# Performance work log

Measured on AMD Instinct MI355X. Metric: run time of the kernel, lower is better.

## Reference

```python
import jax, jax.numpy as jnp
import numpy as np

N = 50000
HEADS = 3
NEG_SLOPE = 0.2


def _add_self_loops(edge_index, num_nodes):
    loops = jnp.arange(num_nodes, dtype=edge_index.dtype)
    return jnp.concatenate([edge_index, jnp.stack([loops, loops])], axis=1)


def _gcn_conv(x, edge_index, W, b):
    # PyG GCNConv: add self loops, symmetric deg^-1/2 normalization.
    ei = _add_self_loops(edge_index, x.shape[0])
    src, dst = ei[0], ei[1]
    deg = jax.ops.segment_sum(jnp.ones_like(dst, dtype=x.dtype), dst, num_segments=x.shape[0])
    dinv = jax.lax.rsqrt(deg)  # deg >= 1 due to self loops
    norm = dinv[src] * dinv[dst]                      # [E']
    xw = x @ W                                        # [N, F_out]
    out = jax.ops.segment_sum(xw[src] * norm[:, None], dst, num_segments=x.shape[0])
    return out + b


def _gat_conv(x, edge_index, W, att_src, att_dst, b):
    # PyG GATConv (concat=True): self loops, per-edge attention, segment softmax.
    n = x.shape[0]
    ei = _add_self_loops(edge_index, n)
    src, dst = ei[0], ei[1]
    h = (x @ W).reshape(n, HEADS, -1)                 # [N, H, C]
    a_s = (h * att_src).sum(-1)                       # [N, H]
    a_d = (h * att_dst).sum(-1)                       # [N, H]
    e = jax.nn.leaky_relu(a_s[src] + a_d[dst], NEG_SLOPE)   # [E', H]
    m = jax.ops.segment_max(e, dst, num_segments=n)   # [N, H] per-dst max
    e = jnp.exp(e - m[dst])
    s = jax.ops.segment_sum(e, dst, num_segments=n)   # [N, H]
    alpha = e / s[dst]                                # [E', H]
    out = jax.ops.segment_sum(h[src] * alpha[:, :, None], dst, num_segments=n)
    return out.reshape(n, -1) + b                     # [N, H*C]


def setup_inputs() -> dict:
    key = jax.random.key(0)
    ks = jax.random.split(key, 9)
    in_ch, out_ch = 256, 64
    hid = 2 * out_ch  # 128
    E = 800000
    x = jax.random.normal(ks[0], (N, in_ch), dtype=jnp.float32)
    edge_index = jax.random.randint(ks[1], (2, E), 0, N, dtype=jnp.int32)
    W1 = jax.random.normal(ks[2], (in_ch, hid), dtype=jnp.float32) / np.sqrt(in_ch)
    b1 = jnp.zeros((hid,), dtype=jnp.float32)
    W2 = jax.random.normal(ks[3], (hid, HEADS * out_ch), dtype=jnp.float32) / np.sqrt(hid)
    att_src = jax.random.normal(ks[4], (HEADS, out_ch), dtype=jnp.float32) / np.sqrt(out_ch)
    att_dst = jax.random.normal(ks[5], (HEADS, out_ch), dtype=jnp.float32) / np.sqrt(out_ch)
    b2 = jnp.zeros((HEADS * out_ch,), dtype=jnp.float32)
    return {"x": x, "edge_index": edge_index, "W1": W1, "b1": b1,
            "W2": W2, "att_src": att_src, "att_dst": att_dst, "b2": b2}


def reference(x, edge_index, W1, b1, W2, att_src, att_dst, b2):
    h = jax.nn.relu(_gcn_conv(x, edge_index, W1, b1))
    # F.dropout(training=False) is identity in eval mode
    h = _gat_conv(h, edge_index, W2, att_src, att_dst, b2)
    return jax.nn.relu(h)
```

## Files before the change

### kernel.cpp

```cpp
#include <hip/hip_runtime.h>
#include <hip/hip_fp16.h>
#include <math.h>

#define NODES    50000
#define IN_CH    256
#define HID      128
#define HEADS    3
#define HC       64
#define OC       (HEADS*HC)
#define NEG_SLOPE 0.2f

typedef _Float16 half8_t __attribute__((ext_vector_type(8)));
typedef _Float16 half4_t __attribute__((ext_vector_type(4)));
typedef float float4_t __attribute__((ext_vector_type(4)));

__device__ __forceinline__ float lrelu(float v) { return v > 0.f ? v : NEG_SLOPE * v; }

__device__ __forceinline__ unsigned fkey(float f) {
    unsigned b = __float_as_uint(f);
    return (b & 0x80000000u) ? ~b : (b | 0x80000000u);
}
__device__ __forceinline__ float fdec(unsigned k) {
    unsigned b = (k & 0x80000000u) ? (k ^ 0x80000000u) : ~k;
    return __uint_as_float(b);
}

__global__ __launch_bounds__(256) void k_hist(const int* __restrict__ dst, int E, int* __restrict__ cnt,
                                              unsigned short* __restrict__ rank,
                                              const float* __restrict__ W1, const float* __restrict__ W2,
                                              _Float16* __restrict__ W1t, _Float16* __restrict__ W2t) {
    int e = blockIdx.x * 256 + threadIdx.x;
    if (e < E) {
        int r = atomicAdd(&cnt[dst[e]], 1);
        rank[e] = (unsigned short)r;
    }
    if (e < IN_CH * HID) {
        int c = e >> 8, k = e & 255;
        W1t[e] = (_Float16)W1[(size_t)k * HID + c];
    } else if (e < IN_CH * HID + HID * OC) {
        int u = e - IN_CH * HID;
        int c = u >> 7, k = u & 127;
        W2t[u] = (_Float16)W2[(size_t)k * OC + c];
    }
}

__global__ __launch_bounds__(1024) void k_scanA(const int* __restrict__ cnt, int* __restrict__ off,
                                                float* __restrict__ dinv, int* __restrict__ bsum, int n) {
    __shared__ int wsums[16];
    int tid = threadIdx.x, lane = tid & 63, wid = tid >> 6;
    int i = blockIdx.x * 1024 + tid;
    int v = (i < n) ? cnt[i] : 0;
    int incl = v;
    #pragma unroll
    for (int d = 1; d < 64; d <<= 1) {
        int t = __shfl_up(incl, d, 64);
        if (lane >= d) incl += t;
    }
    if (lane == 63) wsums[wid] = incl;
    __syncthreads();
    if (tid == 0) {
        int run = 0;
        #pragma unroll
        for (int j = 0; j < 16; j++) { int t = wsums[j]; wsums[j] = run; run += t; }
        bsum[blockIdx.x] = run;
    }
    __syncthreads();
    if (i < n) {
        off[i] = wsums[wid] + incl - v;
        dinv[i] = rsqrtf((float)(v + 1));
    }
}

__global__ __launch_bounds__(64) void k_scanB(const int* __restrict__ bsum, int* __restrict__ bbase,
                                              int* __restrict__ off, int nb, int n) {
    int tid = threadIdx.x;
    int v = (tid < nb) ? bsum[tid] : 0;
    int incl = v;
    #pragma unroll
    for (int d = 1; d < 64; d <<= 1) {
        int t = __shfl_up(incl, d, 64);
        if (tid >= d) incl += t;
    }
    bbase[tid] = incl - v;
    if (tid == 63) off[n] = incl;
}

__global__ __launch_bounds__(256) void k_scanC(int* __restrict__ off, const int* __restrict__ bbase, int n) {
    int i = blockIdx.x * 256 + threadIdx.x;
    if (i < n) off[i] += bbase[i >> 10];
}

__global__ __launch_bounds__(256) void k_fillg1(const int* __restrict__ src, const int* __restrict__ dst, int E,
                                                const int* __restrict__ off, const unsigned short* __restrict__ rank,
                                                unsigned short* __restrict__ csr,
                                                const float* __restrict__ x, const _Float16* __restrict__ W1t,
                                                const float* __restrict__ dinv, _Float16* __restrict__ xwh,
                                                int n, int fillBlocks) {
    if ((int)blockIdx.x < fillBlocks) {
        int e = blockIdx.x * 256 + threadIdx.x;
        if (e < E) {
            int d = dst[e];
            int p = off[d] + (int)rank[e];
            csr[p] = (unsigned short)src[e];
        }
        return;
    }

    int bid = blockIdx.x - fillBlocks;
    int wid = threadIdx.x >> 6, lane = threadIdx.x & 63;
    int lrow = lane & 15, kgrp = lane >> 4;
    int arow = bid * 64 + wid * 16 + lrow;
    bool rv = arow < n;
    const float* xp = x + (size_t)arow * IN_CH + kgrp * 8;

    float4_t acc[8];
    #pragma unroll
    for (int s = 0; s < 8; s++) acc[s] = (float4_t)(0.f);

    #pragma unroll
    for (int kc = 0; kc < IN_CH; kc += 32) {
        float4 a0, a1;
        if (rv) { a0 = *(const float4*)(xp + kc); a1 = *(const float4*)(xp + kc + 4); }
        else { a0 = make_float4(0.f,0.f,0.f,0.f); a1 = a0; }
        half8_t af;
        af[0]=(_Float16)a0.x; af[1]=(_Float16)a0.y; af[2]=(_Float16)a0.z; af[3]=(_Float16)a0.w;
        af[4]=(_Float16)a1.x; af[5]=(_Float16)a1.y; af[6]=(_Float16)a1.z; af[7]=(_Float16)a1.w;
        #pragma unroll
        for (int s = 0; s < 8; s++) {
            const _Float16* bp = W1t + (size_t)(s * 16 + lrow) * IN_CH + kc + kgrp * 8;
            half8_t bf = *(const half8_t*)bp;
            acc[s] = __builtin_amdgcn_mfma_f32_16x16x32_f16(af, bf, acc[s], 0, 0, 0);
        }
    }

    int orow0 = bid * 64 + wid * 16 + kgrp * 4;
    #pragma unroll
    for (int r = 0; r < 4; r++) {
        int orow = orow0 + r;
        if (orow < n) {
            float sc = dinv[orow];
            _Float16* po = xwh + ((size_t)orow << 7) + lrow;
            #pragma unroll
            for (int s = 0; s < 8; s++) po[s * 16] = (_Float16)(sc * acc[s][r]);
        }
    }
}

__global__ __launch_bounds__(256) void k_gcn(const _Float16* __restrict__ xwh, const unsigned short* __restrict__ csr,
                                             const int* __restrict__ off, const float* __restrict__ dinv,
                                             const float* __restrict__ b1, _Float16* __restrict__ hh, int n) {
    int w = (blockIdx.x * 256 + threadIdx.x) >> 6;
    int lane = threadIdx.x & 63;
    if (w >= n) return;
    int egrp = lane >> 4;
    int c8 = (lane & 15) * 8;
    float acc[8];
    #pragma unroll
    for (int j = 0; j < 8; j++) acc[j] = 0.f;

    int beg = off[w], end = off[w + 1];
    int i = beg;
    for (; i + 16 <= end; i += 16) {
        int s0 = csr[i + egrp];
        int s1 = csr[i + 4 + egrp];
        int s2 = csr[i + 8 + egrp];
        int s3 = csr[i + 12 + egrp];
        half8_t v0 = *(const half8_t*)(xwh + ((size_t)s0 << 7) + c8);
        half8_t v1 = *(const half8_t*)(xwh + ((size_t)s1 << 7) + c8);
        half8_t v2 = *(const half8_t*)(xwh + ((size_t)s2 << 7) + c8);
        half8_t v3 = *(const half8_t*)(xwh + ((size_t)s3 << 7) + c8);
        half8_t p01 = v0 + v1;
        half8_t p23 = v2 + v3;
        #pragma unroll
        for (int j = 0; j < 8; j++)
            acc[j] += (float)p01[j] + (float)p23[j];
    }
    for (; i + 4 <= end; i += 4) {
        int s = csr[i + egrp];
        half8_t v = *(const half8_t*)(xwh + ((size_t)s << 7) + c8);
        #pragma unroll
        for (int j = 0; j < 8; j++) acc[j] += (float)v[j];
    }
    if (i < end && egrp < (end - i)) {
        int s = csr[i + egrp];
        half8_t v = *(const half8_t*)(xwh + ((size_t)s << 7) + c8);
        #pragma unroll
        for (int j = 0; j < 8; j++) acc[j] += (float)v[j];
    }

    #pragma unroll
    for (int j = 0; j < 8; j++) {
        acc[j] += __shfl_xor(acc[j], 16, 64);
        acc[j] += __shfl_xor(acc[j], 32, 64);
    }
    if (egrp == 0) {
        float di = dinv[w];
        half8_t self = *(const half8_t*)(xwh + ((size_t)w << 7) + c8);
        float4 bb0 = *(const float4*)(b1 + c8);
        float4 bb1 = *(const float4*)(b1 + c8 + 4);
        float bv[8] = {bb0.x, bb0.y, bb0.z, bb0.w, bb1.x, bb1.y, bb1.z, bb1.w};
        half8_t o;
        #pragma unroll
        for (int j = 0; j < 8; j++)
            o[j] = (_Float16)fmaxf(fmaf(di, acc[j] + (float)self[j], bv[j]), 0.f);
        *(half8_t*)(hh + ((size_t)w << 7) + c8) = o;
    }
}

__global__ __launch_bounds__(256) void k_gemm2att(const _Float16* __restrict__ hh, const _Float16* __restrict__ W2t,
                                                  const float* __restrict__ att_s, const float* __restrict__ att_d,
                                                  _Float16* __restrict__ h2h, float* __restrict__ a_s4,
                                                  float* __restrict__ a_d4, int n) {
    __shared__ _Float16 hs2[64][200];
    int wid = threadIdx.x >> 6, lane = threadIdx.x & 63;
    int lrow = lane & 15, kgrp = lane >> 4;
    int arow = blockIdx.x * 64 + wid * 16 + lrow;
    bool rv = arow < n;
    const _Float16* hp = hh + ((size_t)arow << 7) + kgrp * 8;

    float4_t acc[12];
    #pragma unroll
    for (int s = 0; s < 12; s++) acc[s] = (float4_t)(0.f);

    #pragma unroll
    for (int kc = 0; kc < HID; kc += 32) {
        half8_t af = (half8_t)((_Float16)0.f);
        if (rv) af = *(const half8_t*)(hp + kc);
        #pragma unroll
        for (int s = 0; s < 12; s++) {
            const _Float16* bp = W2t + (size_t)(s * 16 + lrow) * HID + kc + kgrp * 8;
            half8_t bf = *(const half8_t*)bp;
            acc[s] = __builtin_amdgcn_mfma_f32_16x16x32_f16(af, bf, acc[s], 0, 0, 0);
        }
    }

    int orow0 = blockIdx.x * 64 + wid * 16 + kgrp * 4;
    #pragma unroll
    for (int r = 0; r < 4; r++) {
        int orow = orow0 + r;
        int rloc = wid * 16 + kgrp * 4 + r;
        if (orow < n) {
            _Float16* po = h2h + (size_t)orow * OC + lrow;
            #pragma unroll
            for (int s = 0; s < 12; s++) {
                _Float16 hv = (_Float16)acc[s][r];
                po[s * 16] = hv;
                hs2[rloc][s * 16 + lrow] = hv;
            }
        } else {
            #pragma unroll
            for (int s = 0; s < 12; s++) hs2[rloc][s * 16 + lrow] = (_Float16)0.f;
        }
    }
    __syncthreads();

    bool act = lane < 48;
    int ll = act ? lane : (lane - 48);
    int hd = ll >> 4;
    int c4 = ll * 4;
    float4 as = *(const float4*)(att_s + c4);
    float4 ad = *(const float4*)(att_d + c4);
    for (int j = 0; j < 16; j++) {
        int rloc = wid * 16 + j;
        int orow = blockIdx.x * 64 + rloc;
        half4_t hv = *(const half4_t*)&hs2[rloc][c4];
        float vs = (float)hv[0] * as.x + (float)hv[1] * as.y + (float)hv[2] * as.z + (float)hv[3] * as.w;
        float vd = (float)hv[0] * ad.x + (float)hv[1] * ad.y + (float)hv[2] * ad.z + (float)hv[3] * ad.w;
        #pragma unroll
        for (int o = 1; o < 16; o <<= 1) {
            vs += __shfl_xor(vs, o, 64);
            vd += __shfl_xor(vd, o, 64);
        }
        if (act && (ll & 15) == 0 && orow < n) {
            a_s4[orow * 4 + hd] = vs;
            a_d4[orow * 4 + hd] = vd;
        }
    }
}

__global__ __launch_bounds__(1024) void k_asmax(const float* __restrict__ a_s4, int n, unsigned* __restrict__ asmaxk) {
    int i = blockIdx.x * 1024 + threadIdx.x;
    float m0 = -1e30f, m1 = -1e30f, m2 = -1e30f;
    if (i < n) {
        float4 v = *(const float4*)(a_s4 + (size_t)i * 4);
        m0 = v.x; m1 = v.y; m2 = v.z;
    }
    #pragma unroll
    for (int o = 32; o > 0; o >>= 1) {
        m0 = fmaxf(m0, __shfl_xor(m0, o, 64));
        m1 = fmaxf(m1, __shfl_xor(m1, o, 64));
        m2 = fmaxf(m2, __shfl_xor(m2, o, 64));
    }
    __shared__ float sm[16][3];
    int lane = threadIdx.x & 63, wid = threadIdx.x >> 6;
    if (lane == 0) { sm[wid][0] = m0; sm[wid][1] = m1; sm[wid][2] = m2; }
    __syncthreads();
    if (threadIdx.x == 0) {
        for (int j = 1; j < 16; j++) {
            m0 = fmaxf(m0, sm[j][0]); m1 = fmaxf(m1, sm[j][1]); m2 = fmaxf(m2, sm[j][2]);
        }
        atomicMax(asmaxk + 0, fkey(m0));
        atomicMax(asmaxk + 1, fkey(m1));
        atomicMax(asmaxk + 2, fkey(m2));
    }
}

#define GAT_EDGE(ev, hv) do { \
    float wl = __expf(lrelu((ev) + adh) - Ch); \
    ssum += wl; \
    a0 = fmaf(wl, (float)(hv)[0], a0); \
    a1 = fmaf(wl, (float)(hv)[1], a1); \
    a2 = fmaf(wl, (float)(hv)[2], a2); \
    a3 = fmaf(wl, (float)(hv)[3], a3); \
} while (0)

__global__ __launch_bounds__(256) void k_gat(const _Float16* __restrict__ h2h, const unsigned short* __restrict__ csr,
                                             const int* __restrict__ off, const float* __restrict__ a_s4,
                                             const float* __restrict__ a_d4, const unsigned* __restrict__ asmaxk,
                                             const float* __restrict__ b2, float* __restrict__ out, int n) {
    int w = (blockIdx.x * 256 + threadIdx.x) >> 6;
    int lane = threadIdx.x & 63;
    if (w >= n) return;
    bool act = lane < 48;
    int ll = act ? lane : (lane - 48);
    int hd = ll >> 4;
    int c4 = ll * 4;

    float adh = a_d4[w * 4 + hd];
    float Ch  = lrelu(fdec(asmaxk[hd]) + adh);
    float ash = a_s4[w * 4 + hd];
    float wsl = __expf(lrelu(ash + adh) - Ch);
    float ssum = wsl;
    half4_t hv = *(const half4_t*)(h2h + (size_t)w * OC + c4);
    float a0 = wsl * (float)hv[0], a1 = wsl * (float)hv[1];
    float a2 = wsl * (float)hv[2], a3 = wsl * (float)hv[3];

    int beg = off[w], end = off[w + 1];
    int i = beg;
    for (; i + 4 <= end; i += 4) {
        int sA = csr[i], sB = csr[i + 1], sC = csr[i + 2], sD = csr[i + 3];
        float eA = a_s4[(size_t)sA * 4 + hd];
        float eB = a_s4[(size_t)sB * 4 + hd];
        float eC = a_s4[(size_t)sC * 4 + hd];
        float eD = a_s4[(size_t)sD * 4 + hd];
        half4_t hA = *(const half4_t*)(h2h + (size_t)sA * OC + c4);
        half4_t hB = *(const half4_t*)(h2h + (size_t)sB * OC + c4);
        half4_t hC = *(const half4_t*)(h2h + (size_t)sC * OC + c4);
        half4_t hD = *(const half4_t*)(h2h + (size_t)sD * OC + c4);
        GAT_EDGE(eA, hA); GAT_EDGE(eB, hB); GAT_EDGE(eC, hC); GAT_EDGE(eD, hD);
    }
    for (; i < end; i++) {
        int s = csr[i];
        float ev = a_s4[(size_t)s * 4 + hd];
        half4_t hx = *(const half4_t*)(h2h + (size_t)s * OC + c4);
        GAT_EDGE(ev, hx);
    }

    if (act) {
        float inv = 1.f / ssum;
        float4 bb = *(const float4*)(b2 + c4);
        float4 o;
        o.x = fmaxf(fmaf(a0, inv, bb.x), 0.f);
        o.y = fmaxf(fmaf(a1, inv, bb.y), 0.f);
        o.z = fmaxf(fmaf(a2, inv, bb.z), 0.f);
        o.w = fmaxf(fmaf(a3, inv, bb.w), 0.f);
        *(float4*)(out + (size_t)w * OC + c4) = o;
    }
}

extern "C" void kernel_launch(void* const* d_in, const int* in_sizes, int n_in,
                              void* d_out, int out_size, void* d_ws, size_t ws_size,
                              hipStream_t stream) {
    const float* x        = (const float*)d_in[0];
    const int*   ei       = (const int*)d_in[1];
    const float* W1       = (const float*)d_in[2];
    const float* b1       = (const float*)d_in[3];
    const float* W2       = (const float*)d_in[4];
    const float* att_src  = (const float*)d_in[5];
    const float* att_dst  = (const float*)d_in[6];
    const float* b2       = (const float*)d_in[7];
    float* out = (float*)d_out;

    const int n = in_sizes[0] / IN_CH;
    const int E = in_sizes[1] / 2;
    const int* src = ei;
    const int* dst = ei + E;

    char* ws = (char*)d_ws;
    int*            cnt    = (int*)(ws + 0);
    unsigned*       asmaxk = (unsigned*)(ws + 200704);
    int*            off    = (int*)(ws + 200960);
    float*          dinv   = (float*)(ws + 401664);
    int*            bsum   = (int*)(ws + 602368);
    int*            bbase  = (int*)(ws + 602624);
    _Float16*       W1t    = (_Float16*)(ws + 602880);
    _Float16*       W2t    = (_Float16*)(ws + 668416);
    unsigned short* csr    = (unsigned short*)(ws + 717568);
    unsigned short* rank   = (unsigned short*)(ws + 2317568);
    float*          a_s4   = (float*)(ws + 3917568);
    float*          a_d4   = (float*)(ws + 4717568);
    _Float16*       xwh    = (_Float16*)(ws + 5517568);
    _Float16*       hh     = (_Float16*)(ws + 18317568);
    _Float16*       h2h    = (_Float16*)(ws + 31117568);

    (void)hipMemsetAsync(ws, 0, 200720, stream);

    int egrid = (E + 255) / 256;
    int nb = (n + 1023) / 1024;
    int gm = (n + 63) / 64;
    k_hist<<<egrid, 256, 0, stream>>>(dst, E, cnt, rank, W1, W2, W1t, W2t);
    k_scanA<<<nb, 1024, 0, stream>>>(cnt, off, dinv, bsum, n);
    k_scanB<<<1, 64, 0, stream>>>(bsum, bbase, off, nb, n);
    k_scanC<<<(n + 255) / 256, 256, 0, stream>>>(off, bbase, n);

    k_fillg1<<<egrid + gm, 256, 0, stream>>>(src, dst, E, off, rank, csr,
                                             x, W1t, dinv, xwh, n, egrid);

    int ngrid = (n + 3) / 4;
    k_gcn<<<ngrid, 256, 0, stream>>>(xwh, csr, off, dinv, b1, hh, n);

    k_gemm2att<<<gm, 256, 0, stream>>>(hh, W2t, att_src, att_dst, h2h, a_s4, a_d4, n);

    k_asmax<<<nb, 1024, 0, stream>>>(a_s4, n, asmaxk);
    k_gat<<<ngrid, 256, 0, stream>>>(h2h, csr, off, a_s4, a_d4, asmaxk, b2, out, n);
}
```

Baseline: 224.8 us.

## Drop scan fixup and asmax kernels by folding them into consumer kernels

The separate pass that adds per-block scan bases to the CSR offsets is removed. Instead, each consumer (CSR fill, GCN and GAT aggregation) adds `bbase[idx>>10]` when it reads an offset, and `off[n]` is set from the last block's local sum. The global max of the source attention logits is now reduced inside `k_gemm2att` with a per-block shared reduction and an atomicMax, so the standalone max kernel goes away. This removes two kernel launches and one pass over the offset and logit arrays, at the cost of one extra small load per offset read.

Result: no change. 226.5 us (+0.7%).

```diff
diff --git a/kernel.cpp b/kernel.cpp
--- a/kernel.cpp
+++ b/kernel.cpp
@@ -82,16 +82,12 @@
         if (tid >= d) incl += t;
     }
     bbase[tid] = incl - v;
-    if (tid == 63) off[n] = incl;
-}
-
-__global__ __launch_bounds__(256) void k_scanC(int* __restrict__ off, const int* __restrict__ bbase, int n) {
-    int i = blockIdx.x * 256 + threadIdx.x;
-    if (i < n) off[i] += bbase[i >> 10];
+    if (tid == nb - 1) off[n] = v;
 }
 
 __global__ __launch_bounds__(256) void k_fillg1(const int* __restrict__ src, const int* __restrict__ dst, int E,
-                                                const int* __restrict__ off, const unsigned short* __restrict__ rank,
+                                                const int* __restrict__ off, const int* __restrict__ bbase,
+                                                const unsigned short* __restrict__ rank,
                                                 unsigned short* __restrict__ csr,
                                                 const float* __restrict__ x, const _Float16* __restrict__ W1t,
                                                 const float* __restrict__ dinv, _Float16* __restrict__ xwh,
@@ -100,7 +96,7 @@
         int e = blockIdx.x * 256 + threadIdx.x;
         if (e < E) {
             int d = dst[e];
-            int p = off[d] + (int)rank[e];
+            int p = off[d] + bbase[d >> 10] + (int)rank[e];
             csr[p] = (unsigned short)src[e];
         }
         return;
@@ -147,7 +143,8 @@
 }
 
 __global__ __launch_bounds__(256) void k_gcn(const _Float16* __restrict__ xwh, const unsigned short* __restrict__ csr,
-                                             const int* __restrict__ off, const float* __restrict__ dinv,
+                                             const int* __restrict__ off, const int* __restrict__ bbase,
+                                             const float* __restrict__ dinv,
                                              const float* __restrict__ b1, _Float16* __restrict__ hh, int n) {
     int w = (blockIdx.x * 256 + threadIdx.x) >> 6;
     int lane = threadIdx.x & 63;
@@ -158,7 +155,8 @@
     #pragma unroll
     for (int j = 0; j < 8; j++) acc[j] = 0.f;
 
-    int beg = off[w], end = off[w + 1];
+    int beg = off[w] + bbase[w >> 10];
+    int end = off[w + 1] + bbase[(w + 1) >> 10];
     int i = beg;
     for (; i + 16 <= end; i += 16) {
         int s0 = csr[i + egrp];
@@ -210,8 +208,9 @@
 __global__ __launch_bounds__(256) void k_gemm2att(const _Float16* __restrict__ hh, const _Float16* __restrict__ W2t,
                                                   const float* __restrict__ att_s, const float* __restrict__ att_d,
                                                   _Float16* __restrict__ h2h, float* __restrict__ a_s4,
-                                                  float* __restrict__ a_d4, int n) {
+                                                  float* __restrict__ a_d4, unsigned* __restrict__ asmaxk, int n) {
     __shared__ _Float16 hs2[64][200];
+    __shared__ float wmax[4][3];
     int wid = threadIdx.x >> 6, lane = threadIdx.x & 63;
     int lrow = lane & 15, kgrp = lane >> 4;
     int arow = blockIdx.x * 64 + wid * 16 + lrow;
@@ -260,6 +259,7 @@
     int c4 = ll * 4;
     float4 as = *(const float4*)(att_s + c4);
     float4 ad = *(const float4*)(att_d + c4);
+    float mx = -1e30f;
     for (int j = 0; j < 16; j++) {
         int rloc = wid * 16 + j;
         int orow = blockIdx.x * 64 + rloc;
@@ -274,34 +274,15 @@
         if (act && (ll & 15) == 0 && orow < n) {
             a_s4[orow * 4 + hd] = vs;
             a_d4[orow * 4 + hd] = vd;
-        }
-    }
-}
-
-__global__ __launch_bounds__(1024) void k_asmax(const float* __restrict__ a_s4, int n, unsigned* __restrict__ asmaxk) {
-    int i = blockIdx.x * 1024 + threadIdx.x;
-    float m0 = -1e30f, m1 = -1e30f, m2 = -1e30f;
-    if (i < n) {
-        float4 v = *(const float4*)(a_s4 + (size_t)i * 4);
-        m0 = v.x; m1 = v.y; m2 = v.z;
-    }
-    #pragma unroll
-    for (int o = 32; o > 0; o >>= 1) {
-        m0 = fmaxf(m0, __shfl_xor(m0, o, 64));
-        m1 = fmaxf(m1, __shfl_xor(m1, o, 64));
-        m2 = fmaxf(m2, __shfl_xor(m2, o, 64));
-    }
-    __shared__ float sm[16][3];
-    int lane = threadIdx.x & 63, wid = threadIdx.x >> 6;
-    if (lane == 0) { sm[wid][0] = m0; sm[wid][1] = m1; sm[wid][2] = m2; }
+            mx = fmaxf(mx, vs);
+        }
+    }
+    if (act && (ll & 15) == 0) wmax[wid][hd] = mx;
     __syncthreads();
-    if (threadIdx.x == 0) {
-        for (int j = 1; j < 16; j++) {
-            m0 = fmaxf(m0, sm[j][0]); m1 = fmaxf(m1, sm[j][1]); m2 = fmaxf(m2, sm[j][2]);
-        }
-        atomicMax(asmaxk + 0, fkey(m0));
-        atomicMax(asmaxk + 1, fkey(m1));
-        atomicMax(asmaxk + 2, fkey(m2));
+    if (threadIdx.x < 3) {
+        float m = fmaxf(fmaxf(wmax[0][threadIdx.x], wmax[1][threadIdx.x]),
+                        fmaxf(wmax[2][threadIdx.x], wmax[3][threadIdx.x]));
+        if (m > -1e29f) atomicMax(asmaxk + threadIdx.x, fkey(m));
     }
 }
 
@@ -315,7 +296,8 @@
 } while (0)
 
 __global__ __launch_bounds__(256) void k_gat(const _Float16* __restrict__ h2h, const unsigned short* __restrict__ csr,
-                                             const int* __restrict__ off, const float* __restrict__ a_s4,
+                                             const int* __restrict__ off, const int* __restrict__ bbase,
+                                             const float* __restrict__ a_s4,
                                              const float* __restrict__ a_d4, const unsigned* __restrict__ asmaxk,
                                              const float* __restrict__ b2, float* __restrict__ out, int n) {
     int w = (blockIdx.x * 256 + threadIdx.x) >> 6;
@@ -335,7 +317,8 @@
     float a0 = wsl * (float)hv[0], a1 = wsl * (float)hv[1];
     float a2 = wsl * (float)hv[2], a3 = wsl * (float)hv[3];
 
-    int beg = off[w], end = off[w + 1];
+    int beg = off[w] + bbase[w >> 10];
+    int end = off[w + 1] + bbase[(w + 1) >> 10];
     int i = beg;
     for (; i + 4 <= end; i += 4) {
         int sA = csr[i], sB = csr[i + 1], sC = csr[i + 2], sD = csr[i + 3];
@@ -411,16 +394,14 @@
     k_hist<<<egrid, 256, 0, stream>>>(dst, E, cnt, rank, W1, W2, W1t, W2t);
     k_scanA<<<nb, 1024, 0, stream>>>(cnt, off, dinv, bsum, n);
     k_scanB<<<1, 64, 0, stream>>>(bsum, bbase, off, nb, n);
-    k_scanC<<<(n + 255) / 256, 256, 0, stream>>>(off, bbase, n);
-
-    k_fillg1<<<egrid + gm, 256, 0, stream>>>(src, dst, E, off, rank, csr,
+
+    k_fillg1<<<egrid + gm, 256, 0, stream>>>(src, dst, E, off, bbase, rank, csr,
                                              x, W1t, dinv, xwh, n, egrid);
 
     int ngrid = (n + 3) / 4;
-    k_gcn<<<ngrid, 256, 0, stream>>>(xwh, csr, off, dinv, b1, hh, n);
-
-    k_gemm2att<<<gm, 256, 0, stream>>>(hh, W2t, att_src, att_dst, h2h, a_s4, a_d4, n);
-
-    k_asmax<<<nb, 1024, 0, stream>>>(a_s4, n, asmaxk);
-    k_gat<<<ngrid, 256, 0, stream>>>(h2h, csr, off, a_s4, a_d4, asmaxk, b2, out, n);
-}
+    k_gcn<<<ngrid, 256, 0, stream>>>(xwh, csr, off, bbase, dinv, b1, hh, n);
+
+    k_gemm2att<<<gm, 256, 0, stream>>>(hh, W2t, att_src, att_dst, h2h, a_s4, a_d4, asmaxk, n);
+
+    k_gat<<<ngrid, 256, 0, stream>>>(h2h, csr, off, bbase, a_s4, a_d4, asmaxk, b2, out, n);
+}
```
